# Kernel optimization log

Measured on AMD Instinct MI355X. Metric: run time of the kernel, lower is better.

Reference implementation:

```python
import jax, jax.numpy as jnp
import numpy as np
from jax import lax

NEG = -1e30  # finite stand-in for -inf so logaddexp grads stay finite


def setup_inputs() -> dict:
    key = jax.random.key(0)
    k1, k2, k3, k4, k5 = jax.random.split(key, 5)
    B, T, L, S = 16, 2048, 256, 8
    return {
        "emissions": jax.random.normal(k1, (B, T, S), dtype=jnp.float32),
        "transition": jax.random.normal(k2, (S, S), dtype=jnp.float32),
        "bos": jax.random.normal(k3, (S,), dtype=jnp.float32),
        "eos": jax.random.normal(k4, (S,), dtype=jnp.float32),
        "lengths": jnp.full((B,), T, dtype=jnp.int32),
        "targets": jax.random.randint(k5, (B, L), 0, 4, dtype=jnp.int32),
        "target_lengths": jnp.full((B,), L, dtype=jnp.int32),
    }


def _den_logz(em, lengths, transition, bos, eos):
    # Exact log-semiring forward over the fully-connected 8-state denominator CRF graph
    # (the limit of k2.intersect_dense_pruned(...).get_tot_scores(log_semiring=True)).
    B, T, S = em.shape
    alpha0 = bos[None, :] + em[:, 0, :]  # (B,S)

    def step(alpha, em_t):
        a = jax.nn.logsumexp(alpha[:, :, None] + transition[None, :, :], axis=1) + em_t
        return a, a

    _, alphas = lax.scan(step, alpha0, jnp.swapaxes(em, 0, 1)[1:])  # (T-1,B,S)
    alphas = jnp.concatenate([alpha0[None], alphas], axis=0)  # (T,B,S)
    fin = alphas[lengths - 1, jnp.arange(B)]  # (B,S) alpha at last valid frame
    return jax.nn.logsumexp(fin + eos[None, :], axis=-1)


def _num_logz(em, lengths, targets, target_lengths, transition, bos, eos):
    # Forward over the target-constrained enter/extend lattice: symbol u must be
    # entered (state targets[u]) exactly once, optionally extended (state targets[u]+4),
    # then the path moves monotonically to symbol u+1.
    B, T, S = em.shape
    L = targets.shape[1]
    b_idx = jnp.arange(B)
    es = targets          # enter-state ids, (B,L)
    xs = targets + 4      # extend-state ids, (B,L)

    t_xx = transition[xs, xs]  # extend_u -> extend_u
    t_ex = transition[es, xs]  # enter_u  -> extend_u
    prev_e = jnp.concatenate([es[:, :1], es[:, :-1]], axis=1)
    prev_x = jnp.concatenate([xs[:, :1], xs[:, :-1]], axis=1)
    t_ee = transition[prev_e, es]  # enter_{u-1}  -> enter_u
    t_xe = transition[prev_x, es]  # extend_{u-1} -> enter_u

    a_e0 = jnp.full((B, L), NEG, dtype=em.dtype)
    a_e0 = a_e0.at[:, 0].set(bos[es[:, 0]] + em[b_idx, 0, es[:, 0]])
    a_x0 = jnp.full((B, L), NEG, dtype=em.dtype)

    def shift(a):  # a[:, u-1], NEG at u=0
        return jnp.concatenate([jnp.full((B, 1), NEG, dtype=a.dtype), a[:, :-1]], axis=1)

    def step(carry, em_t):
        a_e, a_x = carry
        em_e = jnp.take_along_axis(em_t, es, axis=1)  # (B,L)
        em_x = jnp.take_along_axis(em_t, xs, axis=1)
        new_e = em_e + jnp.logaddexp(shift(a_e) + t_ee, shift(a_x) + t_xe)
        new_x = em_x + jnp.logaddexp(a_e + t_ex, a_x + t_xx)
        return (new_e, new_x), (new_e, new_x)

    _, (ae, ax) = lax.scan(step, (a_e0, a_x0), jnp.swapaxes(em, 0, 1)[1:])
    ae = jnp.concatenate([a_e0[None], ae], axis=0)  # (T,B,L)
    ax = jnp.concatenate([a_x0[None], ax], axis=0)
    fin_e = ae[lengths - 1, b_idx]  # (B,L)
    fin_x = ax[lengths - 1, b_idx]
    u = target_lengths - 1
    fe = fin_e[b_idx, u] + eos[es[b_idx, u]]
    fx = fin_x[b_idx, u] + eos[xs[b_idx, u]]
    return jnp.logaddexp(fe, fx)  # (B,)


def reference(emissions, transition, bos, eos, lengths, targets, target_lengths):
    em = emissions.astype(jnp.float32)
    logz_den = _den_logz(em, lengths, transition, bos, eos)
    logz_num = _num_logz(em, lengths, targets, target_lengths, transition, bos, eos)
    # all samples valid by construction (lengths > 0, 0 < target_len <= length)
    return jnp.mean(logz_den - logz_num)
```

## Files before the change

### kernel.cpp

```cpp
#include <hip/hip_runtime.h>
#include <math.h>


#define LOG2E 1.4426950408889634f
#define LN2   0.69314718055994531f
#define CTL_WSHL1  0x130
#define CTL_WSHR1  0x138
#define CTL_ROR(r) (0x120 + (r))

#define AST(p, v) __hip_atomic_store((p), (v), __ATOMIC_RELAXED, __HIP_MEMORY_SCOPE_AGENT)
#define ALD(p)    __hip_atomic_load((p), __ATOMIC_RELAXED, __HIP_MEMORY_SCOPE_AGENT)

template <int CTRL>
__device__ __forceinline__ float fdpp(float x) {
    return __int_as_float(__builtin_amdgcn_update_dpp(
        0, __float_as_int(x), CTRL, 0xF, 0xF, true));
}
template <int CTRL>
__device__ __forceinline__ int idpp(int x) {
    return __builtin_amdgcn_update_dpp(0, x, CTRL, 0xF, 0xF, true);
}

__device__ __forceinline__ void pin() {
#if __has_builtin(__builtin_amdgcn_sched_barrier)
    __builtin_amdgcn_sched_barrier(0);
#else
    asm volatile("" ::: "memory");
#endif
}

__device__ __forceinline__ float fexp2(float x) {
#if __has_builtin(__builtin_amdgcn_exp2f)
    return __builtin_amdgcn_exp2f(x);
#else
    return exp2f(x);
#endif
}
__device__ __forceinline__ float flog2(float x) {
#if __has_builtin(__builtin_amdgcn_logf)
    return __builtin_amdgcn_logf(x);
#else
    return __log2f(x);
#endif
}
__device__ __forceinline__ float lse2(float a, float b) {
    float m = fmaxf(a, b);
    float d = fminf(a, b) - m;
    return m + flog2(1.0f + fexp2(d));
}

#define NFW_STEP {                                                          \
    float2 q0 = st0[tb + k + 1], q1 = st1[tb + k + 1];                      \
    float2 rv = make_float2(0.0f, 0.0f);                                    \
    if (CONS) rv = rEX[k * 64 + 63];                                        \
    float nbE = fdpp<CTL_WSHR1>(E[1]);                                      \
    float nbX = fdpp<CTL_WSHR1>(X[1]);                                      \
    if (CONS && l0) { nbE = rv.x; nbX = rv.y; }                             \
    float nE0 = p0.x * fmaf(nbE,  teeF, nbX  * txeF);                       \
    float nE1 = p1.x * fmaf(E[0], tee1, X[0] * txe1);                       \
    float nX0 = p0.y * fmaf(E[0], tex0, X[0] * txx0);                       \
    float nX1 = p1.y * fmaf(E[1], tex1, X[1] * txx1);                       \
    E[0] = nE0; E[1] = nE1; X[0] = nX0; X[1] = nX1;                         \
    if (!CONS) rEX[(k + 1) * 64 + lane] = make_float2(E[1], X[1]);          \
    if ((k & 7) == 7) {                                                     \
        int rs = 0;                                                         \
        if (CONS) rs = rS[(k >> 3) * 64 + 63];                              \
        float m = fmaxf(fmaxf(E[0], E[1]), fmaxf(X[0], X[1]));              \
        const bool live = (m > 0.0f);                                       \
        const int ex = live ? ((int)(__float_as_uint(m) >> 23) - 126) : 0;  \
        s += ex;                                                            \
        int bs = idpp<CTL_WSHR1>(s);                                        \
        if (CONS && l0) bs = rs;                                            \
        if (!live) s = bs;                                                  \
        int d = (g == 0) ? 0 : (bs - s);                                    \
        const int extra = (d > 30) ? d : 0;                                 \
        s += extra; d -= extra;                                             \
        const float fsc = ldexpf(1.0f, -(ex + extra));                      \
        E[0] *= fsc; E[1] *= fsc; X[0] *= fsc; X[1] *= fsc;                 \
        const float fs0 = (g == 0) ? 0.0f : ldexpf(1.0f, d);                \
        teeF = tee0 * fs0; txeF = txe0 * fs0;                               \
        if (!CONS) { rS[(k >> 3) * 64 + lane] = s;                          \
                     rEX[(k + 1) * 64 + lane] = make_float2(E[1], X[1]); }  \
    }                                                                       \
    p0 = q0; p1 = q1; }

template <bool CONS>
__device__ __forceinline__ void nfwd_chunk(
    const float2* st0, const float2* st1,
    float (&E)[2], float (&X)[2], int& s, float& teeF, float& txeF,
    float tee0, float txe0, float tee1, float txe1,
    float tex0, float txx0, float tex1, float txx1,
    int tb, int n, int g, int lane, float2* rEX, int* rS)
{
    const bool l0 = (lane == 0);
    if (!CONS) rEX[lane] = make_float2(E[1], X[1]);
    float2 p0 = st0[tb], p1 = st1[tb];
    if (n == 16) {
#pragma unroll
        for (int k = 0; k < 16; ++k) NFW_STEP
    } else {
        for (int k = 0; k < n; ++k) NFW_STEP
    }
}

#define NBW_STEP {                                                          \
    float2 q0 = st0[tb - k - 1], q1 = st1[tb - k - 1];                      \
    float rm = 0.0f;                                                        \
    if (CONS) rm = rM[k * 64];                                              \
    float mm0 = p0.x * bE[0];                                               \
    float mm1 = p1.x * bE[1];                                               \
    float m10 = p0.y * bX[0];                                               \
    float m11 = p1.y * bX[1];                                               \
    float mup = fdpp<CTL_WSHL1>(mm0);                                       \
    if (CONS && l63) mup = rm;                                              \
    if (!CONS) rM[k * 64 + lane] = mm0;                                     \
    float nE0 = fmaf(tex0, m10, teeN0 * mm1);                               \
    float nX0 = fmaf(txx0, m10, txeN0 * mm1);                               \
    float nE1 = fmaf(tex1, m11, teeN1F * mup);                              \
    float nX1 = fmaf(txx1, m11, txeN1F * mup);                              \
    bE[0] = nE0; bE[1] = nE1; bX[0] = nX0; bX[1] = nX1;                     \
    if ((k & 7) == 7) {                                                     \
        int rs = 0;                                                         \
        if (CONS) rs = rS[(k >> 3) * 64];                                   \
        float m = fmaxf(fmaxf(bE[0], bE[1]), fmaxf(bX[0], bX[1]));          \
        const bool live = (m > 0.0f);                                       \
        const int ex = live ? ((int)(__float_as_uint(m) >> 23) - 126) : 0;  \
        s += ex;                                                            \
        int bs = idpp<CTL_WSHL1>(s);                                        \
        if (CONS && l63) bs = rs;                                           \
        if (!live) s = bs;                                                  \
        int d = (g == 127) ? 0 : (bs - s);                                  \
        const int extra = (d > 30) ? d : 0;                                 \
        s += extra; d -= extra;                                             \
        const float fsc = ldexpf(1.0f, -(ex + extra));                      \
        bE[0] *= fsc; bE[1] *= fsc; bX[0] *= fsc; bX[1] *= fsc;             \
        const float fs = (g == 127) ? 0.0f : ldexpf(1.0f, d);               \
        teeN1F = teeN1 * fs; txeN1F = txeN1 * fs;                           \
        if (!CONS) rS[(k >> 3) * 64 + lane] = s;                            \
    }                                                                       \
    p0 = q0; p1 = q1; }

template <bool CONS>
__device__ __forceinline__ void nbwd_chunk(
    const float2* st0, const float2* st1,
    float (&bE)[2], float (&bX)[2], int& s, float& teeN1F, float& txeN1F,
    float teeN0, float txeN0, float teeN1, float txeN1,
    float tex0, float txx0, float tex1, float txx1,
    int tb, int n, int g, int lane, float* rM, int* rS)
{
    const bool l63 = (lane == 63);
    float2 p0 = st0[tb], p1 = st1[tb];
    if (n == 16) {
#pragma unroll
        for (int k = 0; k < 16; ++k) NBW_STEP
    } else {
        for (int k = 0; k < n; ++k) NBW_STEP
    }
}

__device__ __forceinline__ float denf_step(float al, float emt, const float* Tr) {
    float v1 = fdpp<CTL_ROR(1)>(al);
    float v2 = fdpp<CTL_ROR(2)>(al);
    float v3 = fdpp<CTL_ROR(3)>(al);
    float v4 = fdpp<CTL_ROR(4)>(al);
    float v5 = fdpp<CTL_ROR(5)>(al);
    float v6 = fdpp<CTL_ROR(6)>(al);
    float v7 = fdpp<CTL_ROR(7)>(al);
    float q0 = fmaf(v1, Tr[1], al * Tr[0]);
    float q1 = fmaf(v3, Tr[3], v2 * Tr[2]);
    float q2 = fmaf(v5, Tr[5], v4 * Tr[4]);
    float q3 = fmaf(v7, Tr[7], v6 * Tr[6]);
    return ((q0 + q1) + (q2 + q3)) * emt;
}
__device__ __forceinline__ float denb_step(float al, float emt, const float* TrB) {
    float g  = al * emt;
    float v1 = fdpp<CTL_ROR(7)>(g);
    float v2 = fdpp<CTL_ROR(6)>(g);
    float v3 = fdpp<CTL_ROR(5)>(g);
    float v4 = fdpp<CTL_ROR(4)>(g);
    float v5 = fdpp<CTL_ROR(3)>(g);
    float v6 = fdpp<CTL_ROR(2)>(g);
    float v7 = fdpp<CTL_ROR(1)>(g);
    float q0 = fmaf(v1, TrB[1], g * TrB[0]);
    float q1 = fmaf(v3, TrB[3], v2 * TrB[2]);
    float q2 = fmaf(v5, TrB[5], v4 * TrB[4]);
    float q3 = fmaf(v7, TrB[7], v6 * TrB[6]);
    return (q0 + q1) + (q2 + q3);
}
__device__ __forceinline__ int den_renorm(float& al) {
    float mm = fmaxf(al, fdpp<CTL_ROR(4)>(al));
    mm = fmaxf(mm, fdpp<CTL_ROR(2)>(mm));
    mm = fmaxf(mm, fdpp<CTL_ROR(1)>(mm));
    const int ex = (int)(__float_as_uint(mm) >> 23) - 126;
    al = ldexpf(al, -ex);
    return ex;
}

extern "C" __global__ void __launch_bounds__(128)
crf_fused(const float* __restrict__ em, const float* __restrict__ trans,
          const float* __restrict__ bos, const float* __restrict__ eos,
          const int* __restrict__ lengths, const int* __restrict__ targets,
          const int* __restrict__ tlens,
          float* __restrict__ ws, float* __restrict__ out,
          int B, int T, int S, int L)
{
    extern __shared__ float sm[];
    const int bid  = blockIdx.x;
    const int tid  = threadIdx.x;
    const int lane = tid & 63;
    const int wv   = tid >> 6;
    const int half = S >> 1;
    const int role = bid / B;
    const int b    = bid % B;
    const float* gem = em + (size_t)b * T * S;
    const int len = lengths[b];
    const int tm  = (len - 1) >> 1;
    const int P2  = T + 2;
    const int RINGF = 8 * P2;

    float* NF  = ws + 16 + (size_t)b * 640;
    float* NB  = ws + 16 + (size_t)B * 640 + (size_t)b * 640;
    const size_t DENR = 16 + (size_t)(2 * B) * 640;
    const size_t MATF = DENR + (size_t)B * 32;
    const size_t MATB = MATF + (size_t)B * 128;
    int* ticket = (int*)ws;

    const int tq  = tm >> 1;
    const int dlo = tm + 1, dhi = len - 1;
    const int tq2 = (dhi >= dlo) ? (dlo + ((dhi - dlo) >> 1)) : (dlo - 1);

    if (role < 2) {
        float2* s2 = (float2*)sm;
        for (int t = tid; t < T; t += 128) {
            const float4* gr = (const float4*)(gem + t * S);
            float4 a = gr[0], c4 = gr[1];
            s2[0 * P2 + t] = make_float2(fexp2(a.x * LOG2E), fexp2(c4.x * LOG2E));
            s2[1 * P2 + t] = make_float2(fexp2(a.y * LOG2E), fexp2(c4.y * LOG2E));
            s2[2 * P2 + t] = make_float2(fexp2(a.z * LOG2E), fexp2(c4.z * LOG2E));
            s2[3 * P2 + t] = make_float2(fexp2(a.w * LOG2E), fexp2(c4.w * LOG2E));
        }
    } else {
        for (int t = tid; t < T; t += 128) {
            const float4* gr = (const float4*)(gem + t * S);
            float4 a = gr[0], c4 = gr[1];
            float4 w0, w1;
            w0.x = fexp2(a.x * LOG2E); w0.y = fexp2(c4.x * LOG2E);
            w0.z = fexp2(a.y * LOG2E); w0.w = fexp2(c4.y * LOG2E);
            w1.x = fexp2(a.z * LOG2E); w1.y = fexp2(c4.z * LOG2E);
            w1.z = fexp2(a.w * LOG2E); w1.w = fexp2(c4.w * LOG2E);
            ((float4*)sm)[t * 2]     = w0;
            ((float4*)sm)[t * 2 + 1] = w1;
        }
    }
    __syncthreads();

    if (role == 0) {
        const float2* s2v = (const float2*)sm;
        const int g   = (wv << 6) + lane;
        const int u0g = g * 2;
        const int base = b * L;
        const int e0 = targets[base + ((u0g     < L) ? u0g     : (L - 1))];
        const int e1 = targets[base + ((u0g + 1 < L) ? u0g + 1 : (L - 1))];
        const int ep = (u0g > 0) ? targets[base + u0g - 1] : e0;
        const float tee0 = fexp2(trans[ep * S + e0] * LOG2E);
        const float txe0 = fexp2(trans[(ep + half) * S + e0] * LOG2E);
        const float tee1 = fexp2(trans[e0 * S + e1] * LOG2E);
        const float txe1 = fexp2(trans[(e0 + half) * S + e1] * LOG2E);
        const float tex0 = fexp2(trans[e0 * S + e0 + half] * LOG2E);
        const float txx0 = fexp2(trans[(e0 + half) * S + e0 + half] * LOG2E);
        const float tex1 = fexp2(trans[e1 * S + e1 + half] * LOG2E);
        const float txx1 = fexp2(trans[(e1 + half) * S + e1 + half] * LOG2E);
        const float2* st0 = s2v + e0 * P2;
        const float2* st1 = s2v + e1 * P2;
        float E[2] = {0.f, 0.f}, X[2] = {0.f, 0.f};
        int s = 0;
        if (g == 0) E[0] = fexp2(bos[e0] * LOG2E) * st0[0].x;
        float teeF = (g == 0) ? 0.0f : tee0;
        float txeF = (g == 0) ? 0.0f : txe0;

        float2* ringEX = (float2*)(sm + RINGF);
        int*    ringS  = (int*)(sm + RINGF + 4352);
        const int NCH = (tm + 15) >> 4;
        for (int ph = 0; ph <= NCH; ++ph) {
            const int ci = (wv == 0) ? ph : ph - 1;
            if (ci >= 0 && ci < NCH) {
                const int tb = 1 + (ci << 4);
                int n = tm - tb + 1; if (n > 16) n = 16;
                float2* rEX = ringEX + (ci & 1) * (17 * 64);
                int*    rS  = ringS  + (ci & 1) * 128;
                if (wv == 0)
                    nfwd_chunk<false>(st0, st1, E, X, s, teeF, txeF,
                                      tee0, txe0, tee1, txe1,
                                      tex0, txx0, tex1, txx1,
                                      tb, n, g, lane, rEX, rS);
                else
                    nfwd_chunk<true>(st0, st1, E, X, s, teeF, txeF,
                                     tee0, txe0, tee1, txe1,
                                     tex0, txx0, tex1, txx1,
                                     tb, n, g, lane, rEX, rS);
            }
            __syncthreads();
        }
        AST(&NF[g * 4 + 0], E[0]);
        AST(&NF[g * 4 + 1], E[1]);
        AST(&NF[g * 4 + 2], X[0]);
        AST(&NF[g * 4 + 3], X[1]);
        AST(&NF[512 + g], __int_as_float(s));
    } else if (role == 1) {
        const float2* s2v = (const float2*)sm;
        const int g   = (wv << 6) + lane;
        const int u0g = g * 2;
        const int base = b * L;
        const int e0 = targets[base + ((u0g     < L) ? u0g     : (L - 1))];
        const int e1 = targets[base + ((u0g + 1 < L) ? u0g + 1 : (L - 1))];
        const int e2 = targets[base + ((u0g + 2 < L) ? u0g + 2 : (L - 1))];
        const float tex0 = fexp2(trans[e0 * S + e0 + half] * LOG2E);
        const float txx0 = fexp2(trans[(e0 + half) * S + e0 + half] * LOG2E);
        const float tex1 = fexp2(trans[e1 * S + e1 + half] * LOG2E);
        const float txx1 = fexp2(trans[(e1 + half) * S + e1 + half] * LOG2E);
        const float teeN0 = fexp2(trans[e0 * S + e1] * LOG2E);
        const float txeN0 = fexp2(trans[(e0 + half) * S + e1] * LOG2E);
        float teeN1 = fexp2(trans[e1 * S + e2] * LOG2E);
        float txeN1 = fexp2(trans[(e1 + half) * S + e2] * LOG2E);
        if (g == 127) { teeN1 = 0.0f; txeN1 = 0.0f; }
        const float2* st0 = s2v + e0 * P2;
        const float2* st1 = s2v + e1 * P2;
        float bE[2] = {0.f, 0.f}, bX[2] = {0.f, 0.f};
        const int uf = tlens[b] - 1;
        if (g == (uf >> 1)) {
            const int kf = uf & 1;
            const int ef = kf ? e1 : e0;
            bE[kf] = fexp2(eos[ef] * LOG2E);
            bX[kf] = fexp2(eos[ef + half] * LOG2E);
        }
        int s = 0;
        float teeN1F = teeN1, txeN1F = txeN1;

        float* ringM = sm + RINGF;
        int*   ringS = (int*)(sm + RINGF + 4352);
        const int th = len - 1, tlo = tm + 1;
        const int nbs = th - tlo + 1;
        const int NCH = (nbs > 0) ? ((nbs + 15) >> 4) : 0;
        for (int ph = 0; ph <= NCH; ++ph) {
            const int ci = (wv == 1) ? ph : ph - 1;
            if (ci >= 0 && ci < NCH) {
                const int tb = th - (ci << 4);
                int n = tb - tlo + 1; if (n > 16) n = 16;
                float* rM = ringM + (ci & 1) * 1024;
                int*   rS = ringS + (ci & 1) * 128;
                if (wv == 1)
                    nbwd_chunk<false>(st0, st1, bE, bX, s, teeN1F, txeN1F,
                                      teeN0, txeN0, teeN1, txeN1,
                                      tex0, txx0, tex1, txx1,
                                      tb, n, g, lane, rM, rS);
                else
                    nbwd_chunk<true>(st0, st1, bE, bX, s, teeN1F, txeN1F,
                                     teeN0, txeN0, teeN1, txeN1,
                                     tex0, txx0, tex1, txx1,
                                     tb, n, g, lane, rM, rS);
            }
            __syncthreads();
        }
        AST(&NB[g * 4 + 0], bE[0]);
        AST(&NB[g * 4 + 1], bE[1]);
        AST(&NB[g * 4 + 2], bX[0]);
        AST(&NB[g * 4 + 3], bX[1]);
        AST(&NB[512 + g], __int_as_float(s));
    } else if (role == 2) {
        float* DR = ws + DENR + (size_t)b * 32;
        const int j  = lane & 7;
        const int jj = ((j & 3) << 1) + (j >> 2);
        if (wv == 0) {
            float Tr[8];
#pragma unroll
            for (int r = 0; r < 8; ++r)
                Tr[r] = fexp2(trans[((j - r) & 7) * S + j] * LOG2E);
            float al = fexp2(bos[j] * LOG2E) * sm[jj];
            int sc = 0;
            int t = 1;
            if (t + 3 <= tq) {
                float c0 = sm[t * 8 + jj];
                float c1 = sm[(t + 1) * 8 + jj];
                float c2 = sm[(t + 2) * 8 + jj];
                float c3 = sm[(t + 3) * 8 + jj];
                pin();
                while (t + 7 <= tq) {
                    float d0 = sm[(t + 4) * 8 + jj];
                    float d1 = sm[(t + 5) * 8 + jj];
                    float d2 = sm[(t + 6) * 8 + jj];
                    float d3 = sm[(t + 7) * 8 + jj];
                    pin();
                    al = denf_step(al, c0, Tr);
                    al = denf_step(al, c1, Tr);
                    al = denf_step(al, c2, Tr);
                    al = denf_step(al, c3, Tr);
                    sc += den_renorm(al);
                    c0 = d0; c1 = d1; c2 = d2; c3 = d3;
                    t += 4;
                }
                al = denf_step(al, c0, Tr);
                al = denf_step(al, c1, Tr);
                al = denf_step(al, c2, Tr);
                al = denf_step(al, c3, Tr);
                sc += den_renorm(al);
                t += 4;
            }
            while (t <= tq) { al = denf_step(al, sm[t * 8 + jj], Tr); ++t; }
            if (lane < 8) {
                AST(&DR[j], al);
                if (j == 0) AST(&DR[8], __int_as_float(sc));
            }
        } else {
            float TrB[8];
#pragma unroll
            for (int r = 0; r < 8; ++r)
                TrB[r] = fexp2(trans[j * S + ((j + r) & 7)] * LOG2E);
            float al = fexp2(eos[j] * LOG2E);
            int sc = 0;
            int t = dhi;
            const int tloR = tq2 + 1;
            if (t - 3 >= tloR) {
                float c0 = sm[t * 8 + jj];
                float c1 = sm[(t - 1) * 8 + jj];
                float c2 = sm[(t - 2) * 8 + jj];
                float c3 = sm[(t - 3) * 8 + jj];
                pin();
                while (t - 7 >= tloR) {
                    float d0 = sm[(t - 4) * 8 + jj];
                    float d1 = sm[(t - 5) * 8 + jj];
                    float d2 = sm[(t - 6) * 8 + jj];
                    float d3 = sm[(t - 7) * 8 + jj];
                    pin();
                    al = denb_step(al, c0, TrB);
                    al = denb_step(al, c1, TrB);
                    al = denb_step(al, c2, TrB);
                    al = denb_step(al, c3, TrB);
                    sc += den_renorm(al);
                    c0 = d0; c1 = d1; c2 = d2; c3 = d3;
                    t -= 4;
                }
                al = denb_step(al, c0, TrB);
                al = denb_step(al, c1, TrB);
                al = denb_step(al, c2, TrB);
                al = denb_step(al, c3, TrB);
                sc += den_renorm(al);
                t -= 4;
            }
            while (t >= tloR) { al = denb_step(al, sm[t * 8 + jj], TrB); --t; }
            if (lane < 8) {
                AST(&DR[16 + j], al);
                if (j == 0) AST(&DR[24], __int_as_float(sc));
            }
        }
    } else if (role == 3) {
        float* MF = ws + MATF + (size_t)b * 128;
        const int j  = lane & 7;
        const int jj = ((j & 3) << 1) + (j >> 2);
        const int cc = (wv << 2) + (lane >> 4);
        float Tr[8];
#pragma unroll
        for (int r = 0; r < 8; ++r)
            Tr[r] = fexp2(trans[((j - r) & 7) * S + j] * LOG2E);
        float al = (j == cc) ? 1.0f : 0.0f;
        int sc = 0;
        int t = tq + 1;
        if (t + 3 <= tm) {
            float c0 = sm[t * 8 + jj];
            float c1 = sm[(t + 1) * 8 + jj];
            float c2 = sm[(t + 2) * 8 + jj];
            float c3 = sm[(t + 3) * 8 + jj];
            pin();
            while (t + 7 <= tm) {
                float d0 = sm[(t + 4) * 8 + jj];
                float d1 = sm[(t + 5) * 8 + jj];
                float d2 = sm[(t + 6) * 8 + jj];
                float d3 = sm[(t + 7) * 8 + jj];
                pin();
                al = denf_step(al, c0, Tr);
                al = denf_step(al, c1, Tr);
                al = denf_step(al, c2, Tr);
                al = denf_step(al, c3, Tr);
                sc += den_renorm(al);
                c0 = d0; c1 = d1; c2 = d2; c3 = d3;
                t += 4;
            }
            al = denf_step(al, c0, Tr);
            al = denf_step(al, c1, Tr);
            al = denf_step(al, c2, Tr);
            al = denf_step(al, c3, Tr);
            sc += den_renorm(al);
            t += 4;
        }
        while (t <= tm) { al = denf_step(al, sm[t * 8 + jj], Tr); ++t; }
        if ((lane & 15) < 8) {
            AST(&MF[cc * 8 + j], al);
            if (j == 0) AST(&MF[64 + cc], __int_as_float(sc));
        }
    } else {
        float* MB = ws + MATB + (size_t)b * 128;
        const int j  = lane & 7;
        const int jj = ((j & 3) << 1) + (j >> 2);
        const int cc = (wv << 2) + (lane >> 4);
        float TrB[8];
#pragma unroll
        for (int r = 0; r < 8; ++r)
            TrB[r] = fexp2(trans[j * S + ((j + r) & 7)] * LOG2E);
        float al = (j == cc) ? 1.0f : 0.0f;
        int sc = 0;
        int t = tq2;
        if (t - 3 >= dlo) {
            float c0 = sm[t * 8 + jj];
            float c1 = sm[(t - 1) * 8 + jj];
            float c2 = sm[(t - 2) * 8 + jj];
            float c3 = sm[(t - 3) * 8 + jj];
            pin();
            while (t - 7 >= dlo) {
                float d0 = sm[(t - 4) * 8 + jj];
                float d1 = sm[(t - 5) * 8 + jj];
                float d2 = sm[(t - 6) * 8 + jj];
                float d3 = sm[(t - 7) * 8 + jj];
                pin();
                al = denb_step(al, c0, TrB);
                al = denb_step(al, c1, TrB);
                al = denb_step(al, c2, TrB);
                al = denb_step(al, c3, TrB);
                sc += den_renorm(al);
                c0 = d0; c1 = d1; c2 = d2; c3 = d3;
                t -= 4;
            }
            al = denb_step(al, c0, TrB);
            al = denb_step(al, c1, TrB);
            al = denb_step(al, c2, TrB);
            al = denb_step(al, c3, TrB);
            sc += den_renorm(al);
            t -= 4;
        }
        while (t >= dlo) { al = denb_step(al, sm[t * 8 + jj], TrB); --t; }
        if ((lane & 15) < 8) {
            AST(&MB[cc * 8 + j], al);
            if (j == 0) AST(&MB[64 + cc], __int_as_float(sc));
        }
    }

    __syncthreads();
    int* wflag = (int*)sm;
    if (tid == 0) {
        __threadfence();
        const int tk = atomicAdd(ticket, 1);
        wflag[0] = (tk == 5 * B - 1) ? 1 : 0;
    }
    __syncthreads();
    if (wflag[0] && tid < 64) {
        __threadfence();
        float acc = 0.0f;
        const int c8 = lane >> 3, j8 = lane & 7;
        for (int bb2 = 0; bb2 < B; ++bb2) {
            const float* nf = ws + 16 + (size_t)bb2 * 640;
            const float* nb = ws + 16 + (size_t)B * 640 + (size_t)bb2 * 640;
            float va = 0.0f, vb = 0.0f;
#pragma unroll
            for (int k = 0; k < 4; ++k)
                va = fmaf(ALD(&nf[lane * 4 + k]), ALD(&nb[lane * 4 + k]), va);
#pragma unroll
            for (int k = 0; k < 4; ++k)
                vb = fmaf(ALD(&nf[256 + lane * 4 + k]),
                          ALD(&nb[256 + lane * 4 + k]), vb);
            const int sa = __float_as_int(ALD(&nf[512 + lane]))
                         + __float_as_int(ALD(&nb[512 + lane]));
            const int sb = __float_as_int(ALD(&nf[576 + lane]))
                         + __float_as_int(ALD(&nb[576 + lane]));
            float pa = (va > 0.0f) ? (flog2(va) + (float)sa) : -3.0e38f;
            float pb = (vb > 0.0f) ? (flog2(vb) + (float)sb) : -3.0e38f;
            float part = lse2(pa, pb);
#pragma unroll
            for (int o = 1; o < 64; o <<= 1)
                part = lse2(part, __shfl_xor(part, o, 64));

            const float* dr = ws + DENR + (size_t)bb2 * 32;
            const float* mf = ws + MATF + (size_t)bb2 * 128;
            const float* mb = ws + MATB + (size_t)bb2 * 128;
            int s1 = __float_as_int(ALD(&mf[64 + c8]));
            int m1 = s1;
#pragma unroll
            for (int o = 8; o < 64; o <<= 1) {
                int oth = __shfl_xor(m1, o, 64);
                m1 = (oth > m1) ? oth : m1;
            }
            int s2 = __float_as_int(ALD(&mb[64 + c8]));
            int m2 = s2;
#pragma unroll
            for (int o = 8; o < 64; o <<= 1) {
                int oth = __shfl_xor(m2, o, 64);
                m2 = (oth > m2) ? oth : m2;
            }
            float t1 = ALD(&dr[c8]) * ALD(&mf[c8 * 8 + j8])
                     * ldexpf(1.0f, s1 - m1);
#pragma unroll
            for (int o = 8; o < 64; o <<= 1) t1 += __shfl_xor(t1, o, 64);
            float t2 = ALD(&dr[16 + c8]) * ALD(&mb[c8 * 8 + j8])
                     * ldexpf(1.0f, s2 - m2);
#pragma unroll
            for (int o = 8; o < 64; o <<= 1) t2 += __shfl_xor(t2, o, 64);
            float pd = t1 * t2;
#pragma unroll
            for (int o = 1; o < 8; o <<= 1) pd += __shfl_xor(pd, o, 64);
            const int scF = __float_as_int(ALD(&dr[8]));
            const int scB = __float_as_int(ALD(&dr[24]));
            float logden = flog2(fmaxf(pd, 1e-37f))
                         + (float)(scF + scB + m1 + m2);
            if (lane == 0) acc += logden - part;
        }
        if (lane == 0) out[0] = acc * (LN2 / (float)B);
    }
}

extern "C" void kernel_launch(void* const* d_in, const int* in_sizes, int n_in,
                              void* d_out, int out_size, void* d_ws, size_t ws_size,
                              hipStream_t stream)
{
    const float* em      = (const float*)d_in[0];
    const float* trans   = (const float*)d_in[1];
    const float* bos     = (const float*)d_in[2];
    const float* eos     = (const float*)d_in[3];
    const int*   lengths = (const int*)d_in[4];
    const int*   targets = (const int*)d_in[5];
    const int*   tlens   = (const int*)d_in[6];
    float* out = (float*)d_out;
    float* ws  = (float*)d_ws;

    const int B  = in_sizes[4];
    const int SS = in_sizes[1];
    int S = 1; while (S * S < SS) ++S;
    const int T = in_sizes[0] / (B * S);
    const int L = in_sizes[5] / B;

    const size_t shmem = (size_t)(8 * (T + 2) + 4352 + 256) * sizeof(float);

    static bool attr_done = false;
    if (!attr_done) {
        (void)hipFuncSetAttribute((const void*)crf_fused,
                                  hipFuncAttributeMaxDynamicSharedMemorySize,
                                  (int)(96 * 1024));
        attr_done = true;
    }

    (void)hipMemsetAsync(ws, 0, 64, stream);
    hipLaunchKernelGGL(crf_fused, dim3(5 * B), dim3(128), shmem, stream,
                       em, trans, bos, eos, lengths, targets, tlens,
                       ws, out, B, T, S, L);
}
```

Measured before the change: 153.1 us.

## Fuse two time steps per numerator lattice update with precomputed transition products

Rewrites the numerator forward and backward recurrences to advance two frames per step, using precomputed pairwise products of transition weights and emission pairs loaded as float4. The aim is to halve the number of sequential cross-lane DPP dependency steps, cut renormalization frequency per frame, and widen shared-memory loads. In exchange each step does more multiplies, register pressure rises, the ring buffers grow to float4 entries with more shared memory, and the odd/even edge handling adds complexity.

```diff
diff --git a/kernel.cpp b/kernel.cpp
--- a/kernel.cpp
+++ b/kernel.cpp
@@ -49,112 +49,277 @@
     return m + flog2(1.0f + fexp2(d));
 }
 
-#define NFW_STEP {                                                          \
-    float2 q0 = st0[tb + k + 1], q1 = st1[tb + k + 1];                      \
-    float2 rv = make_float2(0.0f, 0.0f);                                    \
-    if (CONS) rv = rEX[k * 64 + 63];                                        \
-    float nbE = fdpp<CTL_WSHR1>(E[1]);                                      \
-    float nbX = fdpp<CTL_WSHR1>(X[1]);                                      \
-    if (CONS && l0) { nbE = rv.x; nbX = rv.y; }                             \
-    float nE0 = p0.x * fmaf(nbE,  teeF, nbX  * txeF);                       \
-    float nE1 = p1.x * fmaf(E[0], tee1, X[0] * txe1);                       \
-    float nX0 = p0.y * fmaf(E[0], tex0, X[0] * txx0);                       \
-    float nX1 = p1.y * fmaf(E[1], tex1, X[1] * txx1);                       \
-    E[0] = nE0; E[1] = nE1; X[0] = nX0; X[1] = nX1;                         \
-    if (!CONS) rEX[(k + 1) * 64 + lane] = make_float2(E[1], X[1]);          \
-    if ((k & 7) == 7) {                                                     \
-        int rs = 0;                                                         \
-        if (CONS) rs = rS[(k >> 3) * 64 + 63];                              \
-        float m = fmaxf(fmaxf(E[0], E[1]), fmaxf(X[0], X[1]));              \
-        const bool live = (m > 0.0f);                                       \
-        const int ex = live ? ((int)(__float_as_uint(m) >> 23) - 126) : 0;  \
-        s += ex;                                                            \
-        int bs = idpp<CTL_WSHR1>(s);                                        \
-        if (CONS && l0) bs = rs;                                            \
-        if (!live) s = bs;                                                  \
-        int d = (g == 0) ? 0 : (bs - s);                                    \
-        const int extra = (d > 30) ? d : 0;                                 \
-        s += extra; d -= extra;                                             \
-        const float fsc = ldexpf(1.0f, -(ex + extra));                      \
-        E[0] *= fsc; E[1] *= fsc; X[0] *= fsc; X[1] *= fsc;                 \
-        const float fs0 = (g == 0) ? 0.0f : ldexpf(1.0f, d);                \
-        teeF = tee0 * fs0; txeF = txe0 * fs0;                               \
-        if (!CONS) { rS[(k >> 3) * 64 + lane] = s;                          \
-                     rEX[(k + 1) * 64 + lane] = make_float2(E[1], X[1]); }  \
-    }                                                                       \
-    p0 = q0; p1 = q1; }
+struct FwdC {
+    float kE0a,kE0b,kE0c,kE0d, kE1a,kE1b,kE1c,kE1d,
+          kX0a,kX0b,kX0c,kX0d, kX1a,kX1b,kX1c,kX1d;
+    float tee0,txe0,tee1,txe1,tex0,txx0,tex1,txx1;
+};
+struct BwdC {
+    float kA,kB,kC,kD,kE,kF,kG,kH,kI,kJ,kK,kL,kM,kN,kO,kP;
+    float tex0,txx0,tex1,txx1,teeN0,txeN0,teeN1,txeN1;
+};
+
 
 template <bool CONS>
-__device__ __forceinline__ void nfwd_chunk(
-    const float2* st0, const float2* st1,
-    float (&E)[2], float (&X)[2], int& s, float& teeF, float& txeF,
-    float tee0, float txe0, float tee1, float txe1,
-    float tex0, float txx0, float tex1, float txx1,
-    int tb, int n, int g, int lane, float2* rEX, int* rS)
-{
-    const bool l0 = (lane == 0);
-    if (!CONS) rEX[lane] = make_float2(E[1], X[1]);
-    float2 p0 = st0[tb], p1 = st1[tb];
-    if (n == 16) {
-#pragma unroll
-        for (int k = 0; k < 16; ++k) NFW_STEP
+__device__ __forceinline__ void fw_single(
+    const float2* f20, const float2* f21, int t,
+    float& E0, float& E1, float& X0, float& X1,
+    float fs0, const FwdC& c, float4* rb, int k, int lane)
+{
+    const float2 p0 = f20[t], p1 = f21[t];
+    float4 rv = make_float4(0.f,0.f,0.f,0.f);
+    if (CONS) rv = rb[k * 64 + 63];
+    float nbE = fdpp<CTL_WSHR1>(E1);
+    float nbX = fdpp<CTL_WSHR1>(X1);
+    if (CONS && lane == 0) { nbE = rv.y; nbX = rv.w; }
+    nbE *= fs0; nbX *= fs0;
+    const float nE0 = p0.x * fmaf(nbE, c.tee0, nbX * c.txe0);
+    const float nE1 = p1.x * fmaf(E0, c.tee1, X0 * c.txe1);
+    const float nX0 = p0.y * fmaf(E0, c.tex0, X0 * c.txx0);
+    const float nX1 = p1.y * fmaf(E1, c.tex1, X1 * c.txx1);
+    E0 = nE0; E1 = nE1; X0 = nX0; X1 = nX1;
+    if (!CONS) rb[(k + 1) * 64 + lane] = make_float4(E0, E1, X0, X1);
+}
+
+template <bool CONS>
+__device__ __forceinline__ void fw_double(
+    const float4* s40, const float4* s41, const float4* s4p, int th2,
+    float& E0, float& E1, float& X0, float& X1,
+    float fs0, const FwdC& c, float4* rb, int k, int lane)
+{
+    const float4 a0 = s40[th2];
+    const float4 a1 = s41[th2];
+    const float4 ap = s4p[th2];
+    float4 rv = make_float4(0.f,0.f,0.f,0.f);
+    if (CONS) rv = rb[k * 64 + 63];
+    const float av = a0.x, cv = a0.y, a2 = a0.z, c2 = a0.w;
+    const float bv = a1.x, dv = a1.y, b2 = a1.z, d2 = a1.w;
+    const float bp = ap.x, dp = ap.y;
+    const float a2bp = a2 * bp, a2dp = a2 * dp, b2a = b2 * av, b2c = b2 * cv,
+                c2a = c2 * av, c2c = c2 * cv, d2b = d2 * bv, d2d = d2 * dv;
+    const float cE0a = a2bp * c.kE0a, cE0b = a2bp * c.kE0b,
+                cE0c = a2dp * c.kE0c, cE0d = a2dp * c.kE0d;
+    const float cE1a = b2a * c.kE1a, cE1b = b2a * c.kE1b,
+                cE1c = b2c * c.kE1c, cE1d = b2c * c.kE1d;
+    const float cX0a = c2a * c.kX0a, cX0b = c2a * c.kX0b,
+                cX0c = c2c * c.kX0c, cX0d = c2c * c.kX0d;
+    const float cX1a = d2b * c.kX1a, cX1b = d2b * c.kX1b,
+                cX1c = d2d * c.kX1c, cX1d = d2d * c.kX1d;
+    float eh0 = fdpp<CTL_WSHR1>(E0), eh1 = fdpp<CTL_WSHR1>(E1);
+    float xh0 = fdpp<CTL_WSHR1>(X0), xh1 = fdpp<CTL_WSHR1>(X1);
+    if (CONS && lane == 0) { eh0 = rv.x; eh1 = rv.y; xh0 = rv.z; xh1 = rv.w; }
+    eh0 *= fs0; eh1 *= fs0; xh0 *= fs0; xh1 *= fs0;
+    const float nE0 = fmaf(cE0a, eh0, cE0b * xh0) + fmaf(cE0c, eh1, cE0d * xh1);
+    const float nE1 = fmaf(cE1a, eh1, cE1b * xh1) + fmaf(cE1c, E0, cE1d * X0);
+    const float nX0 = fmaf(cX0a, eh1, cX0b * xh1) + fmaf(cX0c, E0, cX0d * X0);
+    const float nX1 = fmaf(cX1a, E0, cX1b * X0) + fmaf(cX1c, E1, cX1d * X1);
+    E0 = nE0; E1 = nE1; X0 = nX0; X1 = nX1;
+    if (!CONS) rb[(k + 1) * 64 + lane] = make_float4(E0, E1, X0, X1);
+}
+
+template <bool CONS>
+__device__ __forceinline__ void fw_renorm(
+    float& E0, float& E1, float& X0, float& X1, int& s, float& fs0,
+    int g, int lane, float4* rb, int k1, int* rs, int slot)
+{
+    int rsv = 0;
+    if (CONS) rsv = rs[slot * 64 + 63];
+    float m = fmaxf(fmaxf(E0, E1), fmaxf(X0, X1));
+    const bool live = (m > 0.0f);
+    const int ex = live ? ((int)(__float_as_uint(m) >> 23) - 126) : 0;
+    s += ex;
+    int bs = idpp<CTL_WSHR1>(s);
+    if (CONS && lane == 0) bs = rsv;
+    if (!live) s = bs;
+    int d = (g == 0) ? 0 : (bs - s);
+    const int extra = (d > 30) ? d : 0;
+    s += extra; d -= extra;
+    const float fsc = ldexpf(1.0f, -(ex + extra));
+    E0 *= fsc; E1 *= fsc; X0 *= fsc; X1 *= fsc;
+    fs0 = (g == 0) ? 0.0f : ldexpf(1.0f, d);
+    if (!CONS) {
+        rs[slot * 64 + lane] = s;
+        rb[k1 * 64 + lane] = make_float4(E0, E1, X0, X1);
+    }
+}
+
+template <bool CONS>
+__device__ __forceinline__ void fw_chunk(
+    const float2* f20, const float2* f21,
+    const float4* s40, const float4* s41, const float4* s4p,
+    float& E0, float& E1, float& X0, float& X1, int& s, float& fs0,
+    const FwdC& c, int g, int lane, float4* rb, int* rs, int tb, int te)
+{
+    if (!CONS) rb[lane] = make_float4(E0, E1, X0, X1);
+    int t = tb, gk = 0;
+    if (t & 1) {
+        fw_single<CONS>(f20, f21, t, E0, E1, X0, X1, fs0, c, rb, gk, lane);
+        ++t; ++gk;
+    }
+    const int nd = (te >= t) ? ((te - t + 1) >> 1) : 0;
+    const int th2 = t >> 1;
+    if (nd == 8) {
+#pragma unroll
+        for (int i = 0; i < 8; ++i) {
+            fw_double<CONS>(s40, s41, s4p, th2 + i, E0, E1, X0, X1, fs0, c, rb, gk + i, lane);
+            if (((gk + i) & 3) == 3)
+                fw_renorm<CONS>(E0, E1, X0, X1, s, fs0, g, lane, rb, gk + i + 1, rs, (gk + i) >> 2);
+        }
+        t += 16; gk += 8;
+    } else if (nd == 7) {
+#pragma unroll
+        for (int i = 0; i < 7; ++i) {
+            fw_double<CONS>(s40, s41, s4p, th2 + i, E0, E1, X0, X1, fs0, c, rb, gk + i, lane);
+            if (((gk + i) & 3) == 3)
+                fw_renorm<CONS>(E0, E1, X0, X1, s, fs0, g, lane, rb, gk + i + 1, rs, (gk + i) >> 2);
+        }
+        t += 14; gk += 7;
     } else {
-        for (int k = 0; k < n; ++k) NFW_STEP
-    }
-}
-
-#define NBW_STEP {                                                          \
-    float2 q0 = st0[tb - k - 1], q1 = st1[tb - k - 1];                      \
-    float rm = 0.0f;                                                        \
-    if (CONS) rm = rM[k * 64];                                              \
-    float mm0 = p0.x * bE[0];                                               \
-    float mm1 = p1.x * bE[1];                                               \
-    float m10 = p0.y * bX[0];                                               \
-    float m11 = p1.y * bX[1];                                               \
-    float mup = fdpp<CTL_WSHL1>(mm0);                                       \
-    if (CONS && l63) mup = rm;                                              \
-    if (!CONS) rM[k * 64 + lane] = mm0;                                     \
-    float nE0 = fmaf(tex0, m10, teeN0 * mm1);                               \
-    float nX0 = fmaf(txx0, m10, txeN0 * mm1);                               \
-    float nE1 = fmaf(tex1, m11, teeN1F * mup);                              \
-    float nX1 = fmaf(txx1, m11, txeN1F * mup);                              \
-    bE[0] = nE0; bE[1] = nE1; bX[0] = nX0; bX[1] = nX1;                     \
-    if ((k & 7) == 7) {                                                     \
-        int rs = 0;                                                         \
-        if (CONS) rs = rS[(k >> 3) * 64];                                   \
-        float m = fmaxf(fmaxf(bE[0], bE[1]), fmaxf(bX[0], bX[1]));          \
-        const bool live = (m > 0.0f);                                       \
-        const int ex = live ? ((int)(__float_as_uint(m) >> 23) - 126) : 0;  \
-        s += ex;                                                            \
-        int bs = idpp<CTL_WSHL1>(s);                                        \
-        if (CONS && l63) bs = rs;                                           \
-        if (!live) s = bs;                                                  \
-        int d = (g == 127) ? 0 : (bs - s);                                  \
-        const int extra = (d > 30) ? d : 0;                                 \
-        s += extra; d -= extra;                                             \
-        const float fsc = ldexpf(1.0f, -(ex + extra));                      \
-        bE[0] *= fsc; bE[1] *= fsc; bX[0] *= fsc; bX[1] *= fsc;             \
-        const float fs = (g == 127) ? 0.0f : ldexpf(1.0f, d);               \
-        teeN1F = teeN1 * fs; txeN1F = txeN1 * fs;                           \
-        if (!CONS) rS[(k >> 3) * 64 + lane] = s;                            \
-    }                                                                       \
-    p0 = q0; p1 = q1; }
+        for (int i = 0; i < nd; ++i) {
+            fw_double<CONS>(s40, s41, s4p, th2 + i, E0, E1, X0, X1, fs0, c, rb, gk + i, lane);
+            if (((gk + i) & 3) == 3)
+                fw_renorm<CONS>(E0, E1, X0, X1, s, fs0, g, lane, rb, gk + i + 1, rs, (gk + i) >> 2);
+        }
+        t += 2 * nd; gk += nd;
+    }
+    if (t <= te) {
+        fw_single<CONS>(f20, f21, t, E0, E1, X0, X1, fs0, c, rb, gk, lane);
+        if ((gk & 3) == 3)
+            fw_renorm<CONS>(E0, E1, X0, X1, s, fs0, g, lane, rb, gk + 1, rs, gk >> 2);
+    }
+}
+
 
 template <bool CONS>
-__device__ __forceinline__ void nbwd_chunk(
-    const float2* st0, const float2* st1,
-    float (&bE)[2], float (&bX)[2], int& s, float& teeN1F, float& txeN1F,
-    float teeN0, float txeN0, float teeN1, float txeN1,
-    float tex0, float txx0, float tex1, float txx1,
-    int tb, int n, int g, int lane, float* rM, int* rS)
-{
-    const bool l63 = (lane == 63);
-    float2 p0 = st0[tb], p1 = st1[tb];
-    if (n == 16) {
-#pragma unroll
-        for (int k = 0; k < 16; ++k) NBW_STEP
+__device__ __forceinline__ void bw_single(
+    const float2* f20, const float2* f21, const float2* f2n, int t,
+    float& bE0, float& bE1, float& bX0, float& bX1,
+    float fs, const BwdC& c, float4* rb, int k, int lane)
+{
+    const float2 p0 = f20[t], p1 = f21[t], pn = f2n[t];
+    float4 rv = make_float4(0.f,0.f,0.f,0.f);
+    if (CONS) rv = rb[k * 64];
+    const float mm0 = p0.x * bE0;
+    float mup = fdpp<CTL_WSHL1>(mm0);
+    if (CONS && lane == 63) mup = pn.x * rv.x;
+    mup *= fs;
+    const float m10 = p0.y * bX0, m11 = p1.y * bX1, mm1 = p1.x * bE1;
+    const float nE0 = fmaf(c.tex0, m10, c.teeN0 * mm1);
+    const float nX0 = fmaf(c.txx0, m10, c.txeN0 * mm1);
+    const float nE1 = fmaf(c.tex1, m11, c.teeN1 * mup);
+    const float nX1 = fmaf(c.txx1, m11, c.txeN1 * mup);
+    bE0 = nE0; bE1 = nE1; bX0 = nX0; bX1 = nX1;
+    if (!CONS) rb[(k + 1) * 64 + lane] = make_float4(bE0, bE1, bX0, bX1);
+}
+
+template <bool CONS>
+__device__ __forceinline__ void bw_double(
+    const float4* s40, const float4* s41, const float4* s4n, const float4* s4n2,
+    int th2, float& bE0, float& bE1, float& bX0, float& bX1,
+    float fs, const BwdC& c, float4* rb, int k, int lane)
+{
+    const float4 a0 = s40[th2];
+    const float4 a1 = s41[th2];
+    const float4 an = s4n[th2];
+    const float4 an2 = s4n2[th2];
+    float4 rv = make_float4(0.f,0.f,0.f,0.f);
+    if (CONS) rv = rb[k * 64];
+    const float av = a0.z, cv = a0.w, a2 = a0.x, c2 = a0.y;
+    const float bv = a1.z, dv = a1.w, b2 = a1.x, d2 = a1.y;
+    const float au = an.z, cu = an.w, a2u = an.x;
+    const float bu = an2.z;
+    const float c2c = c2 * cv, c2b = c2 * bv, b2d = b2 * dv, b2au = b2 * au,
+                d2d = d2 * dv, d2au = d2 * au, a2ucu = a2u * cu, a2ubu = a2u * bu;
+    const float cE0x0 = c2c * c.kA, cE0e1 = c2b * c.kB,
+                cE0x1 = b2d * c.kC, cE0e0u = b2au * c.kD;
+    const float cX0x0 = c2c * c.kE, cX0e1 = c2b * c.kF,
+                cX0x1 = b2d * c.kG, cX0e0u = b2au * c.kH;
+    const float cE1x1 = d2d * c.kI, cE1e0u = d2au * c.kJ,
+                cE1x0u = a2ucu * c.kK, cE1e1u = a2ubu * c.kL;
+    const float cX1x1 = d2d * c.kM, cX1e0u = d2au * c.kN,
+                cX1x0u = a2ucu * c.kO, cX1e1u = a2ubu * c.kP;
+    float e0u = fdpp<CTL_WSHL1>(bE0);
+    float x0u = fdpp<CTL_WSHL1>(bX0);
+    float e1u = fdpp<CTL_WSHL1>(bE1);
+    if (CONS && lane == 63) { e0u = rv.x; e1u = rv.y; x0u = rv.z; }
+    e0u *= fs; x0u *= fs; e1u *= fs;
+    const float nE0 = fmaf(cE0x0, bX0, cE0e1 * bE1) + fmaf(cE0x1, bX1, cE0e0u * e0u);
+    const float nX0 = fmaf(cX0x0, bX0, cX0e1 * bE1) + fmaf(cX0x1, bX1, cX0e0u * e0u);
+    const float nE1 = fmaf(cE1x1, bX1, cE1e0u * e0u) + fmaf(cE1x0u, x0u, cE1e1u * e1u);
+    const float nX1 = fmaf(cX1x1, bX1, cX1e0u * e0u) + fmaf(cX1x0u, x0u, cX1e1u * e1u);
+    bE0 = nE0; bE1 = nE1; bX0 = nX0; bX1 = nX1;
+    if (!CONS) rb[(k + 1) * 64 + lane] = make_float4(bE0, bE1, bX0, bX1);
+}
+
+template <bool CONS>
+__device__ __forceinline__ void bw_renorm(
+    float& bE0, float& bE1, float& bX0, float& bX1, int& s, float& fs,
+    int g, int lane, float4* rb, int k1, int* rs, int slot)
+{
+    int rsv = 0;
+    if (CONS) rsv = rs[slot * 64];
+    float m = fmaxf(fmaxf(bE0, bE1), fmaxf(bX0, bX1));
+    const bool live = (m > 0.0f);
+    const int ex = live ? ((int)(__float_as_uint(m) >> 23) - 126) : 0;
+    s += ex;
+    int bs = idpp<CTL_WSHL1>(s);
+    if (CONS && lane == 63) bs = rsv;
+    if (!live) s = bs;
+    int d = (g == 127) ? 0 : (bs - s);
+    const int extra = (d > 30) ? d : 0;
+    s += extra; d -= extra;
+    const float fsc = ldexpf(1.0f, -(ex + extra));
+    bE0 *= fsc; bE1 *= fsc; bX0 *= fsc; bX1 *= fsc;
+    fs = (g == 127) ? 0.0f : ldexpf(1.0f, d);
+    if (!CONS) {
+        rs[slot * 64 + lane] = s;
+        rb[k1 * 64 + lane] = make_float4(bE0, bE1, bX0, bX1);
+    }
+}
+
+template <bool CONS>
+__device__ __forceinline__ void bw_chunk(
+    const float2* f20, const float2* f21, const float2* f2n,
+    const float4* s40, const float4* s41, const float4* s4n, const float4* s4n2,
+    float& bE0, float& bE1, float& bX0, float& bX1, int& s, float& fs,
+    const BwdC& c, int g, int lane, float4* rb, int* rs, int tbh, int tbl)
+{
+    if (!CONS) rb[lane] = make_float4(bE0, bE1, bX0, bX1);
+    int t = tbh, gk = 0;
+    if (!(t & 1)) {
+        bw_single<CONS>(f20, f21, f2n, t, bE0, bE1, bX0, bX1, fs, c, rb, gk, lane);
+        --t; ++gk;
+    }
+    const int nd = (t >= tbl) ? ((t - tbl + 1) >> 1) : 0;
+    const int th2 = t >> 1;
+    if (nd == 8) {
+#pragma unroll
+        for (int i = 0; i < 8; ++i) {
+            bw_double<CONS>(s40, s41, s4n, s4n2, th2 - i, bE0, bE1, bX0, bX1, fs, c, rb, gk + i, lane);
+            if (((gk + i) & 3) == 3)
+                bw_renorm<CONS>(bE0, bE1, bX0, bX1, s, fs, g, lane, rb, gk + i + 1, rs, (gk + i) >> 2);
+        }
+        t -= 16; gk += 8;
+    } else if (nd == 7) {
+#pragma unroll
+        for (int i = 0; i < 7; ++i) {
+            bw_double<CONS>(s40, s41, s4n, s4n2, th2 - i, bE0, bE1, bX0, bX1, fs, c, rb, gk + i, lane);
+            if (((gk + i) & 3) == 3)
+                bw_renorm<CONS>(bE0, bE1, bX0, bX1, s, fs, g, lane, rb, gk + i + 1, rs, (gk + i) >> 2);
+        }
+        t -= 14; gk += 7;
     } else {
-        for (int k = 0; k < n; ++k) NBW_STEP
+        for (int i = 0; i < nd; ++i) {
+            bw_double<CONS>(s40, s41, s4n, s4n2, th2 - i, bE0, bE1, bX0, bX1, fs, c, rb, gk + i, lane);
+            if (((gk + i) & 3) == 3)
+                bw_renorm<CONS>(bE0, bE1, bX0, bX1, s, fs, g, lane, rb, gk + i + 1, rs, (gk + i) >> 2);
+        }
+        t -= 2 * nd; gk += nd;
+    }
+    if (t >= tbl) {
+        bw_single<CONS>(f20, f21, f2n, t, bE0, bE1, bX0, bX1, fs, c, rb, gk, lane);
+        if ((gk & 3) == 3)
+            bw_renorm<CONS>(bE0, bE1, bX0, bX1, s, fs, g, lane, rb, gk + 1, rs, gk >> 2);
     }
 }
 
@@ -196,6 +361,8 @@
     return ex;
 }
 
+#define WXP(i, j) fexp2(trans[(i) * S + (j)] * LOG2E)
+
 extern "C" __global__ void __launch_bounds__(128)
 crf_fused(const float* __restrict__ em, const float* __restrict__ trans,
           const float* __restrict__ bos, const float* __restrict__ eos,
@@ -254,117 +421,130 @@
     }
     __syncthreads();
 
+    float4* ring4 = (float4*)(sm + RINGF);
+    int*    ringSB = (int*)(sm + RINGF + 5120);
+
     if (role == 0) {
         const float2* s2v = (const float2*)sm;
         const int g   = (wv << 6) + lane;
-        const int u0g = g * 2;
+        const int u0 = g * 2;
         const int base = b * L;
-        const int e0 = targets[base + ((u0g     < L) ? u0g     : (L - 1))];
-        const int e1 = targets[base + ((u0g + 1 < L) ? u0g + 1 : (L - 1))];
-        const int ep = (u0g > 0) ? targets[base + u0g - 1] : e0;
-        const float tee0 = fexp2(trans[ep * S + e0] * LOG2E);
-        const float txe0 = fexp2(trans[(ep + half) * S + e0] * LOG2E);
-        const float tee1 = fexp2(trans[e0 * S + e1] * LOG2E);
-        const float txe1 = fexp2(trans[(e0 + half) * S + e1] * LOG2E);
-        const float tex0 = fexp2(trans[e0 * S + e0 + half] * LOG2E);
-        const float txx0 = fexp2(trans[(e0 + half) * S + e0 + half] * LOG2E);
-        const float tex1 = fexp2(trans[e1 * S + e1 + half] * LOG2E);
-        const float txx1 = fexp2(trans[(e1 + half) * S + e1 + half] * LOG2E);
-        const float2* st0 = s2v + e0 * P2;
-        const float2* st1 = s2v + e1 * P2;
-        float E[2] = {0.f, 0.f}, X[2] = {0.f, 0.f};
+        const int e0 = targets[base + ((u0     < L) ? u0     : (L - 1))];
+        const int e1 = targets[base + ((u0 + 1 < L) ? u0 + 1 : (L - 1))];
+        const int ep  = (u0 > 0) ? targets[base + u0 - 1] : e0;
+        const int e0p = (u0 > 1) ? targets[base + u0 - 2] : e0;
+        FwdC c;
+        c.tee0 = WXP(ep, e0);          c.txe0 = WXP(ep + half, e0);
+        c.tee1 = WXP(e0, e1);          c.txe1 = WXP(e0 + half, e1);
+        c.tex0 = WXP(e0, e0 + half);   c.txx0 = WXP(e0 + half, e0 + half);
+        c.tex1 = WXP(e1, e1 + half);   c.txx1 = WXP(e1 + half, e1 + half);
+        const float tee1p = WXP(e0p, ep);        const float txe1p = WXP(e0p + half, ep);
+        const float tex1p = WXP(ep, ep + half);  const float txx1p = WXP(ep + half, ep + half);
+        c.kE0a = c.tee0 * tee1p; c.kE0b = c.tee0 * txe1p;
+        c.kE0c = c.txe0 * tex1p; c.kE0d = c.txe0 * txx1p;
+        c.kE1a = c.tee1 * c.tee0; c.kE1b = c.tee1 * c.txe0;
+        c.kE1c = c.txe1 * c.tex0; c.kE1d = c.txe1 * c.txx0;
+        c.kX0a = c.tex0 * c.tee0; c.kX0b = c.tex0 * c.txe0;
+        c.kX0c = c.txx0 * c.tex0; c.kX0d = c.txx0 * c.txx0;
+        c.kX1a = c.tex1 * c.tee1; c.kX1b = c.tex1 * c.txe1;
+        c.kX1c = c.txx1 * c.tex1; c.kX1d = c.txx1 * c.txx1;
+        const float2* f20 = s2v + e0 * P2;
+        const float2* f21 = s2v + e1 * P2;
+        const float4* s40 = (const float4*)f20;
+        const float4* s41 = (const float4*)f21;
+        const float4* s4p = (const float4*)(s2v + ep * P2);
+        float E0 = 0.f, E1 = 0.f, X0 = 0.f, X1 = 0.f;
         int s = 0;
-        if (g == 0) E[0] = fexp2(bos[e0] * LOG2E) * st0[0].x;
-        float teeF = (g == 0) ? 0.0f : tee0;
-        float txeF = (g == 0) ? 0.0f : txe0;
-
-        float2* ringEX = (float2*)(sm + RINGF);
-        int*    ringS  = (int*)(sm + RINGF + 4352);
-        const int NCH = (tm + 15) >> 4;
+        if (g == 0) E0 = fexp2(bos[e0] * LOG2E) * f20[0].x;
+        float fs0 = (g == 0) ? 0.0f : 1.0f;
+
+        const int NCH = (tm >= 1) ? ((tm >> 4) + 1) : 0;
         for (int ph = 0; ph <= NCH; ++ph) {
             const int ci = (wv == 0) ? ph : ph - 1;
             if (ci >= 0 && ci < NCH) {
-                const int tb = 1 + (ci << 4);
-                int n = tm - tb + 1; if (n > 16) n = 16;
-                float2* rEX = ringEX + (ci & 1) * (17 * 64);
-                int*    rS  = ringS  + (ci & 1) * 128;
+                const int tb = (ci == 0) ? 1 : (ci << 4);
+                int te = (ci << 4) + 15; if (te > tm) te = tm;
+                float4* rb = ring4 + (ci & 1) * (10 * 64);
+                int*    rs = ringSB + (ci & 1) * 128;
                 if (wv == 0)
-                    nfwd_chunk<false>(st0, st1, E, X, s, teeF, txeF,
-                                      tee0, txe0, tee1, txe1,
-                                      tex0, txx0, tex1, txx1,
-                                      tb, n, g, lane, rEX, rS);
+                    fw_chunk<false>(f20, f21, s40, s41, s4p,
+                                    E0, E1, X0, X1, s, fs0, c, g, lane, rb, rs, tb, te);
                 else
-                    nfwd_chunk<true>(st0, st1, E, X, s, teeF, txeF,
-                                     tee0, txe0, tee1, txe1,
-                                     tex0, txx0, tex1, txx1,
-                                     tb, n, g, lane, rEX, rS);
+                    fw_chunk<true>(f20, f21, s40, s41, s4p,
+                                   E0, E1, X0, X1, s, fs0, c, g, lane, rb, rs, tb, te);
             }
             __syncthreads();
         }
-        AST(&NF[g * 4 + 0], E[0]);
-        AST(&NF[g * 4 + 1], E[1]);
-        AST(&NF[g * 4 + 2], X[0]);
-        AST(&NF[g * 4 + 3], X[1]);
+        AST(&NF[g * 4 + 0], E0);
+        AST(&NF[g * 4 + 1], E1);
+        AST(&NF[g * 4 + 2], X0);
+        AST(&NF[g * 4 + 3], X1);
         AST(&NF[512 + g], __int_as_float(s));
     } else if (role == 1) {
         const float2* s2v = (const float2*)sm;
         const int g   = (wv << 6) + lane;
-        const int u0g = g * 2;
+        const int u0 = g * 2;
         const int base = b * L;
-        const int e0 = targets[base + ((u0g     < L) ? u0g     : (L - 1))];
-        const int e1 = targets[base + ((u0g + 1 < L) ? u0g + 1 : (L - 1))];
-        const int e2 = targets[base + ((u0g + 2 < L) ? u0g + 2 : (L - 1))];
-        const float tex0 = fexp2(trans[e0 * S + e0 + half] * LOG2E);
-        const float txx0 = fexp2(trans[(e0 + half) * S + e0 + half] * LOG2E);
-        const float tex1 = fexp2(trans[e1 * S + e1 + half] * LOG2E);
-        const float txx1 = fexp2(trans[(e1 + half) * S + e1 + half] * LOG2E);
-        const float teeN0 = fexp2(trans[e0 * S + e1] * LOG2E);
-        const float txeN0 = fexp2(trans[(e0 + half) * S + e1] * LOG2E);
-        float teeN1 = fexp2(trans[e1 * S + e2] * LOG2E);
-        float txeN1 = fexp2(trans[(e1 + half) * S + e2] * LOG2E);
-        if (g == 127) { teeN1 = 0.0f; txeN1 = 0.0f; }
-        const float2* st0 = s2v + e0 * P2;
-        const float2* st1 = s2v + e1 * P2;
-        float bE[2] = {0.f, 0.f}, bX[2] = {0.f, 0.f};
+        const int e0 = targets[base + ((u0     < L) ? u0     : (L - 1))];
+        const int e1 = targets[base + ((u0 + 1 < L) ? u0 + 1 : (L - 1))];
+        const int e2 = targets[base + ((u0 + 2 < L) ? u0 + 2 : (L - 1))];
+        const int e3 = targets[base + ((u0 + 3 < L) ? u0 + 3 : (L - 1))];
+        BwdC c;
+        c.tex0 = WXP(e0, e0 + half);  c.txx0 = WXP(e0 + half, e0 + half);
+        c.tex1 = WXP(e1, e1 + half);  c.txx1 = WXP(e1 + half, e1 + half);
+        c.teeN0 = WXP(e0, e1);        c.txeN0 = WXP(e0 + half, e1);
+        c.teeN1 = WXP(e1, e2);        c.txeN1 = WXP(e1 + half, e2);
+        const float tex0n = WXP(e2, e2 + half);
+        const float teeN0n = WXP(e2, e3);
+        c.kA = c.tex0 * c.txx0;  c.kB = c.tex0 * c.txeN0;
+        c.kC = c.teeN0 * c.tex1; c.kD = c.teeN0 * c.teeN1;
+        c.kE = c.txx0 * c.txx0;  c.kF = c.txx0 * c.txeN0;
+        c.kG = c.txeN0 * c.tex1; c.kH = c.txeN0 * c.teeN1;
+        c.kI = c.tex1 * c.txx1;  c.kJ = c.tex1 * c.txeN1;
+        c.kK = c.teeN1 * tex0n;  c.kL = c.teeN1 * teeN0n;
+        c.kM = c.txx1 * c.txx1;  c.kN = c.txx1 * c.txeN1;
+        c.kO = c.txeN1 * tex0n;  c.kP = c.txeN1 * teeN0n;
+        const float2* f20 = s2v + e0 * P2;
+        const float2* f21 = s2v + e1 * P2;
+        const float2* f2n = s2v + e2 * P2;
+        const float4* s40 = (const float4*)f20;
+        const float4* s41 = (const float4*)f21;
+        const float4* s4n = (const float4*)f2n;
+        const float4* s4n2 = (const float4*)(s2v + e3 * P2);
+        float bE0 = 0.f, bE1 = 0.f, bX0 = 0.f, bX1 = 0.f;
         const int uf = tlens[b] - 1;
         if (g == (uf >> 1)) {
             const int kf = uf & 1;
             const int ef = kf ? e1 : e0;
-            bE[kf] = fexp2(eos[ef] * LOG2E);
-            bX[kf] = fexp2(eos[ef + half] * LOG2E);
+            if (kf) { bE1 = fexp2(eos[ef] * LOG2E); bX1 = fexp2(eos[ef + half] * LOG2E); }
+            else    { bE0 = fexp2(eos[ef] * LOG2E); bX0 = fexp2(eos[ef + half] * LOG2E); }
         }
         int s = 0;
-        float teeN1F = teeN1, txeN1F = txeN1;
-
-        float* ringM = sm + RINGF;
-        int*   ringS = (int*)(sm + RINGF + 4352);
+        float fs = (g == 127) ? 0.0f : 1.0f;
+
         const int th = len - 1, tlo = tm + 1;
         const int nbs = th - tlo + 1;
         const int NCH = (nbs > 0) ? ((nbs + 15) >> 4) : 0;
         for (int ph = 0; ph <= NCH; ++ph) {
             const int ci = (wv == 1) ? ph : ph - 1;
             if (ci >= 0 && ci < NCH) {
-                const int tb = th - (ci << 4);
-                int n = tb - tlo + 1; if (n > 16) n = 16;
-                float* rM = ringM + (ci & 1) * 1024;
-                int*   rS = ringS + (ci & 1) * 128;
+                const int tbh = th - (ci << 4);
+                int tbl = tbh - 15; if (tbl < tlo) tbl = tlo;
+                float4* rb = ring4 + (ci & 1) * (10 * 64);
+                int*    rs = ringSB + (ci & 1) * 128;
                 if (wv == 1)
-                    nbwd_chunk<false>(st0, st1, bE, bX, s, teeN1F, txeN1F,
-                                      teeN0, txeN0, teeN1, txeN1,
-                                      tex0, txx0, tex1, txx1,
-                                      tb, n, g, lane, rM, rS);
+                    bw_chunk<false>(f20, f21, f2n, s40, s41, s4n, s4n2,
+                                    bE0, bE1, bX0, bX1, s, fs, c, g, lane, rb, rs, tbh, tbl);
                 else
-                    nbwd_chunk<true>(st0, st1, bE, bX, s, teeN1F, txeN1F,
-                                     teeN0, txeN0, teeN1, txeN1,
-                                     tex0, txx0, tex1, txx1,
-                                     tb, n, g, lane, rM, rS);
+                    bw_chunk<true>(f20, f21, f2n, s40, s41, s4n, s4n2,
+                                   bE0, bE1, bX0, bX1, s, fs, c, g, lane, rb, rs, tbh, tbl);
             }
             __syncthreads();
         }
-        AST(&NB[g * 4 + 0], bE[0]);
-        AST(&NB[g * 4 + 1], bE[1]);
-        AST(&NB[g * 4 + 2], bX[0]);
-        AST(&NB[g * 4 + 3], bX[1]);
+        AST(&NB[g * 4 + 0], bE0);
+        AST(&NB[g * 4 + 1], bE1);
+        AST(&NB[g * 4 + 2], bX0);
+        AST(&NB[g * 4 + 3], bX1);
         AST(&NB[512 + g], __int_as_float(s));
     } else if (role == 2) {
         float* DR = ws + DENR + (size_t)b * 32;
@@ -634,7 +814,7 @@
     const int T = in_sizes[0] / (B * S);
     const int L = in_sizes[5] / B;
 
-    const size_t shmem = (size_t)(8 * (T + 2) + 4352 + 256) * sizeof(float);
+    const size_t shmem = (size_t)(8 * (T + 2) + 5120 + 256) * sizeof(float);
 
     static bool attr_done = false;
     if (!attr_done) {
```

Result: slower. 196.4 us (+28.3%).
